# Performance work log

Hardware: AMD Instinct MI355X
Metric: run time of the kernel (lower is better)

## Reference

```python
import jax, jax.numpy as jnp
import numpy as np

N = 50000      # nodes
E = 800000     # edges (before self-loops)
F_IN = 128     # num_node_features
H = 4          # heads
C = 32         # graph_hidden_channels (per head)
HC = H * C     # 128
NHID = 512
NOUT = 768
G = 256        # graphs in batch
NEG_SLOPE = 0.2


def setup_inputs() -> dict:
    key = jax.random.key(0)
    ks = jax.random.split(key, 32)
    s = 0.05
    inp = {
        "x": jax.random.normal(ks[0], (N, F_IN), jnp.float32),
        "edge_index": jax.random.randint(ks[1], (2, E), 0, N, jnp.int64),
        "batch": jnp.sort(jax.random.randint(ks[2], (N,), 0, G, jnp.int64)),
    }
    dims = [F_IN, HC, HC]
    k = 3
    for i, din in enumerate(dims, start=1):
        inp[f"w{i}"] = jax.random.normal(ks[k], (din, HC), jnp.float32) * s; k += 1
        inp[f"as{i}"] = jax.random.normal(ks[k], (H, C), jnp.float32) * s; k += 1
        inp[f"ad{i}"] = jax.random.normal(ks[k], (H, C), jnp.float32) * s; k += 1
        inp[f"b{i}"] = jnp.zeros((HC,), jnp.float32)
        inp[f"sk{i}w"] = jax.random.normal(ks[k], (din, HC), jnp.float32) * s; k += 1
        inp[f"sk{i}b"] = jnp.zeros((HC,), jnp.float32)
    inp["m1w"] = jax.random.normal(ks[k], (HC, NHID), jnp.float32) * s; k += 1
    inp["m1b"] = jnp.zeros((NHID,), jnp.float32)
    inp["m2w"] = jax.random.normal(ks[k], (NHID, NOUT), jnp.float32) * s
    inp["m2b"] = jnp.zeros((NOUT,), jnp.float32)
    return inp


def _gat_conv(x, src, dst, W, a_src, a_dst, b):
    # x: [N, din]; src/dst: [E+N] (self-loops included)
    n = x.shape[0]
    h = (x @ W).reshape(n, H, C)                       # [N, H, C]
    e_src = jnp.sum(h * a_src, axis=-1)                # [N, H]
    e_dst = jnp.sum(h * a_dst, axis=-1)                # [N, H]
    e = jax.nn.leaky_relu(e_src[src] + e_dst[dst], NEG_SLOPE)  # [E', H]
    m = jax.ops.segment_max(e, dst, num_segments=n)    # segment softmax (stable)
    ex = jnp.exp(e - m[dst])
    z = jax.ops.segment_sum(ex, dst, num_segments=n)
    alpha = ex / z[dst]                                # [E', H]
    out = jax.ops.segment_sum(alpha[:, :, None] * h[src], dst, num_segments=n)
    return out.reshape(n, HC) + b


def reference(x, edge_index, batch,
              w1, as1, ad1, b1, sk1w, sk1b,
              w2, as2, ad2, b2, sk2w, sk2b,
              w3, as3, ad3, b3, sk3w, sk3b,
              m1w, m1b, m2w, m2b):
    n = x.shape[0]
    loops = jnp.arange(n, dtype=edge_index.dtype)
    src = jnp.concatenate([edge_index[0], loops])      # PyG add_self_loops=True
    dst = jnp.concatenate([edge_index[1], loops])

    h = jax.nn.relu(x @ sk1w + sk1b + _gat_conv(x, src, dst, w1, as1, ad1, b1))
    h = jax.nn.relu(h @ sk2w + sk2b + _gat_conv(h, src, dst, w2, as2, ad2, b2))
    h = jax.nn.relu(h @ sk3w + sk3b + _gat_conv(h, src, dst, w3, as3, ad3, b3))

    pooled = jax.ops.segment_max(h, batch, num_segments=G)  # global_max_pool
    pooled = jnp.where(jnp.isfinite(pooled), pooled, 0.0)   # guard empty graphs
    out = jax.nn.relu(pooled @ m1w + m1b)
    out = out @ m2w + m2b
    return out
```

## Files before the change

kernel.cpp:

```cpp
#include <hip/hip_runtime.h>
#include <hip/hip_bf16.h>
#include <math.h>

#define NN 50000
#define EE 800000
#define EPE 850000
#define HCC 128
#define GGR 256
#define NHIDD 512
#define NOUTD 768
#define CHUNK 256
#define CPAD (CHUNK + 8)
#define SCAN_NBLK ((NN + 1023) / 1024)
#define MBLK ((NN + 63) / 64)
#define NPAD 50176
#define NREP 8
#define NPART (NN / 8)

typedef __attribute__((ext_vector_type(8))) short bf16x8;
typedef __attribute__((ext_vector_type(4))) float f32x4;

__device__ __forceinline__ void atomicMaxF(float* addr, float v) {
    if (v >= 0.f) atomicMax(reinterpret_cast<int*>(addr), __float_as_int(v));
    else atomicMin(reinterpret_cast<unsigned int*>(addr), __float_as_uint(v));
}

__device__ __forceinline__ float lrelu(float x) { return x > 0.f ? x : 0.2f * x; }

__device__ __forceinline__ ushort f2bf(float f) {
    unsigned u = __float_as_uint(f);
    unsigned r = (u + 0x7fffu + ((u >> 16) & 1u)) >> 16;
    return (ushort)r;
}
__device__ __forceinline__ float bf2f(ushort b) {
    return __uint_as_float(((unsigned)b) << 16);
}

__global__ void conv_x(const float* __restrict__ X, ushort* __restrict__ Xb) {
    int i = blockIdx.x * 256 + threadIdx.x;
    if (i < NN * HCC / 4) {
        float4 v = reinterpret_cast<const float4*>(X)[i];
        ushort4 o;
        o.x = f2bf(v.x); o.y = f2bf(v.y); o.z = f2bf(v.z); o.w = f2bf(v.w);
        reinterpret_cast<ushort4*>(Xb)[i] = o;
    }
}

__global__ void conv_w(const float* __restrict__ W, const float* __restrict__ SKW,
                       ushort* __restrict__ Wt) {
    int i = blockIdx.x * 256 + threadIdx.x;
    if (i >= 256 * 128) return;
    int n = i >> 7, k = i & 127;
    float v = (n < 128) ? W[(size_t)k * 128 + n] : SKW[(size_t)k * 128 + (n - 128)];
    Wt[i] = f2bf(v);
}

__global__ void hist_zero8(int* __restrict__ cnt8) {
    int i = blockIdx.x * 256 + threadIdx.x;
    if (i < NREP * NPAD) cnt8[i] = 0;
}

__global__ void hist8(const int* __restrict__ ei, int* __restrict__ cnt8) {
    int e = blockIdx.x * 256 + threadIdx.x;
    if (e >= EPE) return;
    int rep = blockIdx.x & 7;
    int d = (e < EE) ? ei[EE + e] : e - EE;
    atomicAdd(&cnt8[rep * NPAD + d], 1);
}

__global__ __launch_bounds__(256) void scan_partial(const int* __restrict__ cnt8,
                                                    int* __restrict__ excl,
                                                    int* __restrict__ blocksums)
{
    __shared__ int s[256];
    const int b = blockIdx.x, t = threadIdx.x;
    const int idx = b * 1024 + t * 4;
    int a[4] = {0, 0, 0, 0};
    #pragma unroll
    for (int j = 0; j < 4; ++j) {
        if (idx + j < NN) {
            int tot = 0;
            #pragma unroll
            for (int r = 0; r < NREP; ++r) tot += cnt8[r * NPAD + idx + j];
            a[j] = tot;
        }
    }
    int sum4 = a[0] + a[1] + a[2] + a[3];
    s[t] = sum4;
    __syncthreads();
    #pragma unroll
    for (int off = 1; off < 256; off <<= 1) {
        int add = (t >= off) ? s[t - off] : 0;
        __syncthreads();
        s[t] += add;
        __syncthreads();
    }
    int e0 = s[t] - sum4;
    if (idx + 0 < NN) excl[idx + 0] = e0;
    if (idx + 1 < NN) excl[idx + 1] = e0 + a[0];
    if (idx + 2 < NN) excl[idx + 2] = e0 + a[0] + a[1];
    if (idx + 3 < NN) excl[idx + 3] = e0 + a[0] + a[1] + a[2];
    if (t == 255) blocksums[b] = s[255];
}

__global__ __launch_bounds__(64) void scan_sums(int* __restrict__ blocksums,
                                                int* __restrict__ blockoffs,
                                                int* __restrict__ row_start)
{
    __shared__ int s[64];
    int t = threadIdx.x;
    int v = (t < SCAN_NBLK) ? blocksums[t] : 0;
    s[t] = v;
    __syncthreads();
    #pragma unroll
    for (int off = 1; off < 64; off <<= 1) {
        int add = (t >= off) ? s[t - off] : 0;
        __syncthreads();
        s[t] += add;
        __syncthreads();
    }
    if (t < SCAN_NBLK) blockoffs[t] = s[t] - v;
    if (t == 63) row_start[NN] = s[63];
}

__global__ void scan_add(const int* __restrict__ excl, const int* __restrict__ blockoffs,
                         int* __restrict__ row_start, int* __restrict__ cursor)
{
    int i = blockIdx.x * 256 + threadIdx.x;
    if (i >= NN) return;
    int v = excl[i] + blockoffs[i >> 10];
    row_start[i] = v;
    cursor[i] = v;
}

__global__ __launch_bounds__(256) void scatter_part(const int* __restrict__ ei,
                                                    int* __restrict__ cursor,
                                                    int* __restrict__ csr_src)
{
    const int p = blockIdx.x & 7;
    const int q = blockIdx.x >> 3;
    const int nq = gridDim.x >> 3;
    const int lo = p * NPART, hi = lo + NPART;
    const int stride = nq * 256;
    for (int e = q * 256 + threadIdx.x; e < EE; e += stride) {
        int d = ei[EE + e];
        if (d >= lo && d < hi) {
            int s = ei[e];
            int pos = atomicAdd(&cursor[d], 1);
            csr_src[pos] = s;
        }
    }
    for (int i = q * 256 + threadIdx.x; i < NPART; i += stride) {
        int d = lo + i;
        int pos = atomicAdd(&cursor[d], 1);
        csr_src[pos] = d;
    }
}

__global__ __launch_bounds__(256) void gemm_mfma(
    const ushort* __restrict__ Xb,
    const ushort* __restrict__ Wt,
    const float* __restrict__ skb, const float* __restrict__ bb,
    const float* __restrict__ as_, const float* __restrict__ ad_,
    ushort* __restrict__ Hout, float* __restrict__ Agg,
    float* __restrict__ esrc, float* __restrict__ edst)
{
    __shared__ ushort Xs[64 * 128];
    __shared__ float sh_es[64][4], sh_ed[64][4];
    const int r0 = blockIdx.x * 64;
    const int tid = threadIdx.x;
    const int w = tid >> 6;
    const int l = tid & 63;
    const int lm = l & 15;
    const int lk = l >> 4;

    #pragma unroll
    for (int it = 0; it < 4; ++it) {
        int slot = it * 256 + tid;
        int row = slot >> 4;
        int bc = (slot & 15) << 4;
        int n = r0 + row;
        bf16x8 v = (bf16x8)(short)0;
        if (n < NN) v = *reinterpret_cast<const bf16x8*>(Xb + (size_t)n * 128 + (bc >> 1));
        *reinterpret_cast<bf16x8*>(reinterpret_cast<char*>(Xs) + row * 256 + (bc ^ ((row & 7) << 4))) = v;
    }
    __syncthreads();

    f32x4 acc[4][4];
    #pragma unroll
    for (int nb = 0; nb < 4; ++nb)
        #pragma unroll
        for (int rf = 0; rf < 4; ++rf)
            acc[nb][rf] = (f32x4){0.f, 0.f, 0.f, 0.f};

    #pragma unroll
    for (int ks = 0; ks < 4; ++ks) {
        bf16x8 a[4];
        #pragma unroll
        for (int rf = 0; rf < 4; ++rf) {
            int row = rf * 16 + lm;
            int bc = (ks * 32 + lk * 8) * 2;
            a[rf] = *reinterpret_cast<const bf16x8*>(
                reinterpret_cast<const char*>(Xs) + row * 256 + (bc ^ ((row & 7) << 4)));
        }
        #pragma unroll
        for (int nb = 0; nb < 4; ++nb) {
            int ncol = (w * 4 + nb) * 16 + lm;
            bf16x8 b = *reinterpret_cast<const bf16x8*>(Wt + (size_t)ncol * 128 + ks * 32 + lk * 8);
            #pragma unroll
            for (int rf = 0; rf < 4; ++rf)
                acc[nb][rf] = __builtin_amdgcn_mfma_f32_16x16x32_bf16(a[rf], b, acc[nb][rf], 0, 0, 0);
        }
    }

    if (w < 2) {
        float asv[4], adv[4];
        #pragma unroll
        for (int nb = 0; nb < 4; ++nb) {
            int ncol = (w * 4 + nb) * 16 + lm;
            asv[nb] = as_[ncol];
            adv[nb] = ad_[ncol];
        }
        #pragma unroll
        for (int rf = 0; rf < 4; ++rf) {
            #pragma unroll
            for (int r = 0; r < 4; ++r) {
                int nl = rf * 16 + lk * 4 + r;
                int n = r0 + nl;
                float es0 = 0.f, es1 = 0.f, ed0 = 0.f, ed1 = 0.f;
                #pragma unroll
                for (int nb = 0; nb < 4; ++nb) {
                    float v = acc[nb][rf][r];
                    int ncol = (w * 4 + nb) * 16 + lm;
                    if (n < NN) Hout[(size_t)n * 128 + ncol] = f2bf(v);
                    if (nb < 2) { es0 = fmaf(v, asv[nb], es0); ed0 = fmaf(v, adv[nb], ed0); }
                    else        { es1 = fmaf(v, asv[nb], es1); ed1 = fmaf(v, adv[nb], ed1); }
                }
                #pragma unroll
                for (int m = 1; m < 16; m <<= 1) {
                    es0 += __shfl_xor(es0, m); ed0 += __shfl_xor(ed0, m);
                    es1 += __shfl_xor(es1, m); ed1 += __shfl_xor(ed1, m);
                }
                if (lm == 0) {
                    sh_es[nl][w * 2 + 0] = es0; sh_ed[nl][w * 2 + 0] = ed0;
                    sh_es[nl][w * 2 + 1] = es1; sh_ed[nl][w * 2 + 1] = ed1;
                }
            }
        }
    } else {
        #pragma unroll
        for (int nb = 0; nb < 4; ++nb) {
            int ncol = (w * 4 + nb) * 16 + lm;
            int c = ncol - 128;
            #pragma unroll
            for (int rf = 0; rf < 4; ++rf) {
                #pragma unroll
                for (int r = 0; r < 4; ++r) {
                    int n = r0 + rf * 16 + lk * 4 + r;
                    if (n >= NN) continue;
                    Agg[(size_t)n * 128 + c] = acc[nb][rf][r] + skb[c] + bb[c];
                }
            }
        }
    }
    __syncthreads();
    if (tid < 256) {
        int nl = tid >> 2, hd = tid & 3;
        int n = r0 + nl;
        if (n < NN) {
            esrc[n * 4 + hd] = sh_es[nl][hd];
            edst[n * 4 + hd] = sh_ed[nl][hd];
        }
    }
}

__global__ __launch_bounds__(128) void gat_aggr(
    const int* __restrict__ row_start, const int* __restrict__ csr_src,
    const float* __restrict__ esrc, const float* __restrict__ edst,
    const ushort* __restrict__ Hb, const float* __restrict__ skipagg,
    ushort* __restrict__ outbuf)
{
    __shared__ int   lsrc[CHUNK];
    __shared__ float lw[4][CPAD];
    __shared__ float shsc[4];
    __shared__ float accbuf[8][HCC];
    const int d = blockIdx.x;
    const int t = threadIdx.x;
    const int hd = t >> 5;
    const int l = t & 31;
    const int slot = t >> 4;
    const int cg = t & 15;
    const int c0 = cg * 8;
    const int ghd = cg >> 2;
    const int r0 = row_start[d], r1 = row_start[d + 1];
    const float4 edv = *reinterpret_cast<const float4*>(edst + (size_t)d * 4);
    float acc[8] = {0.f, 0.f, 0.f, 0.f, 0.f, 0.f, 0.f, 0.f};
    float m_h = -INFINITY, z_h = 0.f;

    for (int base = r0; base < r1; base += CHUNK) {
        const int nc = min(CHUNK, r1 - base);
        __syncthreads();
        for (int i = t; i < nc; i += 128) {
            int s = csr_src[base + i];
            lsrc[i] = s;
            float4 ev = *reinterpret_cast<const float4*>(esrc + (size_t)s * 4);
            lw[0][i] = lrelu(ev.x + edv.x);
            lw[1][i] = lrelu(ev.y + edv.y);
            lw[2][i] = lrelu(ev.z + edv.z);
            lw[3][i] = lrelu(ev.w + edv.w);
        }
        __syncthreads();
        float mx = m_h;
        for (int i = l; i < nc; i += 32) mx = fmaxf(mx, lw[hd][i]);
        #pragma unroll
        for (int off = 16; off > 0; off >>= 1) mx = fmaxf(mx, __shfl_xor(mx, off, 32));
        float sc = __expf(m_h - mx);
        float zp = 0.f;
        for (int i = l; i < nc; i += 32) {
            float w = __expf(lw[hd][i] - mx);
            lw[hd][i] = w;
            zp += w;
        }
        #pragma unroll
        for (int off = 16; off > 0; off >>= 1) zp += __shfl_xor(zp, off, 32);
        z_h = z_h * sc + zp;
        m_h = mx;
        if (l == 0) shsc[hd] = sc;
        __syncthreads();
        float scg = shsc[ghd];
        #pragma unroll
        for (int j = 0; j < 8; ++j) acc[j] *= scg;
        for (int i = slot; i < nc; i += 8) {
            int s = lsrc[i];
            float wgt = lw[ghd][i];
            bf16x8 row = *reinterpret_cast<const bf16x8*>(Hb + (size_t)s * 128 + c0);
            #pragma unroll
            for (int j = 0; j < 8; ++j)
                acc[j] = fmaf(wgt, bf2f((ushort)row[j]), acc[j]);
        }
    }
    #pragma unroll
    for (int j = 0; j < 8; ++j) accbuf[slot][c0 + j] = acc[j];
    __syncthreads();
    float tot = 0.f;
    #pragma unroll
    for (int s = 0; s < 8; ++s) tot += accbuf[s][t];
    float res = skipagg[(size_t)d * 128 + t] + tot / z_h;
    outbuf[(size_t)d * 128 + t] = f2bf(fmaxf(res, 0.f));
}

__global__ void pool_init(float* __restrict__ pooled) {
    int i = blockIdx.x * 256 + threadIdx.x;
    if (i < GGR * HCC) pooled[i] = -INFINITY;
}

__global__ __launch_bounds__(256) void pool_max_sorted(
    const ushort* __restrict__ xf, const int* __restrict__ batch,
    float* __restrict__ pooled)
{
    __shared__ int gb[32];
    const int n0 = blockIdx.x * 32;
    const int t = threadIdx.x;
    if (t < 32) gb[t] = (n0 + t < NN) ? batch[n0 + t] : -1;
    __syncthreads();
    const int c = t & 127;
    const int half = t >> 7;
    int curg = -1;
    float curv = -INFINITY;
    #pragma unroll 4
    for (int i = 0; i < 16; ++i) {
        int n = n0 + half * 16 + i;
        if (n >= NN) break;
        int g = gb[half * 16 + i];
        float v = bf2f(xf[(size_t)n * 128 + c]);
        if (g != curg) {
            if (curg >= 0) atomicMaxF(&pooled[curg * 128 + c], curv);
            curg = g; curv = v;
        } else {
            curv = fmaxf(curv, v);
        }
    }
    if (curg >= 0) atomicMaxF(&pooled[curg * 128 + c], curv);
}

__global__ __launch_bounds__(512) void mlp1(const float* __restrict__ pooled,
                                            const float* __restrict__ w,
                                            const float* __restrict__ bias,
                                            float* __restrict__ hid)
{
    __shared__ float xs[128];
    int g = blockIdx.x, t = threadIdx.x;
    if (t < 128) {
        float v = pooled[g * 128 + t];
        if (!isfinite(v)) v = 0.f;
        xs[t] = v;
    }
    __syncthreads();
    float acc = 0.f;
    #pragma unroll 8
    for (int k = 0; k < 128; ++k) acc += xs[k] * w[(size_t)k * NHIDD + t];
    hid[(size_t)g * NHIDD + t] = fmaxf(acc + bias[t], 0.f);
}

__global__ __launch_bounds__(768) void mlp2(const float* __restrict__ hid,
                                            const float* __restrict__ w,
                                            const float* __restrict__ bias,
                                            float* __restrict__ out)
{
    __shared__ float xs[NHIDD];
    int g = blockIdx.x, t = threadIdx.x;
    if (t < NHIDD) xs[t] = hid[(size_t)g * NHIDD + t];
    __syncthreads();
    float acc = 0.f;
    #pragma unroll 8
    for (int k = 0; k < NHIDD; ++k) acc += xs[k] * w[(size_t)k * NOUTD + t];
    out[(size_t)g * NOUTD + t] = acc + bias[t];
}

extern "C" void kernel_launch(void* const* d_in, const int* in_sizes, int n_in,
                              void* d_out, int out_size, void* d_ws, size_t ws_size,
                              hipStream_t stream)
{
    const float* x = (const float*)d_in[0];
    const int* ei = (const int*)d_in[1];
    const int* batch = (const int*)d_in[2];
    const float* W[3]   = {(const float*)d_in[3],  (const float*)d_in[9],  (const float*)d_in[15]};
    const float* AS[3]  = {(const float*)d_in[4],  (const float*)d_in[10], (const float*)d_in[16]};
    const float* AD[3]  = {(const float*)d_in[5],  (const float*)d_in[11], (const float*)d_in[17]};
    const float* B[3]   = {(const float*)d_in[6],  (const float*)d_in[12], (const float*)d_in[18]};
    const float* SKW[3] = {(const float*)d_in[7],  (const float*)d_in[13], (const float*)d_in[19]};
    const float* SKB[3] = {(const float*)d_in[8],  (const float*)d_in[14], (const float*)d_in[20]};
    const float* m1w = (const float*)d_in[21];
    const float* m1b = (const float*)d_in[22];
    const float* m2w = (const float*)d_in[23];
    const float* m2b = (const float*)d_in[24];
    float* out = (float*)d_out;

    float* p = (float*)d_ws;
    ushort* bufA = (ushort*)p; p += (size_t)NN * HCC / 2;
    ushort* bufB = (ushort*)p; p += (size_t)NN * HCC / 2;
    ushort* xb   = (ushort*)p; p += (size_t)NN * HCC / 2;
    ushort* hbuf = (ushort*)p; p += (size_t)NN * HCC / 2;
    ushort* wt3  = (ushort*)p; p += 3 * 256 * 128 / 2;
    float* agg  = p; p += (size_t)NN * HCC;
    float* esrc = p; p += NN * 4;
    float* edst = p; p += NN * 4;
    float* pooled = p; p += GGR * HCC;
    float* hidden = p; p += GGR * NHIDD;
    int* cnt8      = (int*)p; p += NREP * NPAD;
    int* cursor    = (int*)p; p += NN;
    int* excl      = (int*)p; p += NN;
    int* row_start = (int*)p; p += NN + 4;
    int* csr_src   = (int*)p; p += EPE;
    int* blocksums = (int*)p; p += 64;
    int* blockoffs = (int*)p; p += 64;

    conv_x<<<(NN * HCC / 4 + 255) / 256, 256, 0, stream>>>(x, xb);
    for (int l = 0; l < 3; ++l)
        conv_w<<<(256 * 128 + 255) / 256, 256, 0, stream>>>(W[l], SKW[l], wt3 + l * 256 * 128);

    hist_zero8<<<(NREP * NPAD + 255) / 256, 256, 0, stream>>>(cnt8);
    hist8<<<(EPE + 255) / 256, 256, 0, stream>>>(ei, cnt8);
    scan_partial<<<SCAN_NBLK, 256, 0, stream>>>(cnt8, excl, blocksums);
    scan_sums<<<1, 64, 0, stream>>>(blocksums, blockoffs, row_start);
    scan_add<<<(NN + 255) / 256, 256, 0, stream>>>(excl, blockoffs, row_start, cursor);
    scatter_part<<<1024, 256, 0, stream>>>(ei, cursor, csr_src);

    const ushort* cur = xb;
    ushort* outs[3] = {bufA, bufB, bufA};
    for (int l = 0; l < 3; ++l) {
        gemm_mfma<<<MBLK, 256, 0, stream>>>(cur, wt3 + l * 256 * 128, SKB[l], B[l],
                                            AS[l], AD[l], hbuf, agg, esrc, edst);
        gat_aggr<<<NN, 128, 0, stream>>>(row_start, csr_src, esrc, edst, hbuf, agg, outs[l]);
        cur = outs[l];
    }
    pool_init<<<(GGR * HCC) / 256, 256, 0, stream>>>(pooled);
    pool_max_sorted<<<(NN + 31) / 32, 256, 0, stream>>>(cur, batch, pooled);
    mlp1<<<GGR, NHIDD, 0, stream>>>(pooled, m1w, m1b, hidden);
    mlp2<<<GGR, NOUTD, 0, stream>>>(hidden, m2w, m2b, out);
}
```

Before: 494.1 us.

## Process one destination node per wavefront in GAT aggregation using shuffles

Replaces the block-per-node GAT aggregation with a wave-per-node kernel, four nodes per 256-thread block. The online softmax is computed in registers over 64-edge chunks with wavefront shuffle reductions, replacing shared-memory staging and block barriers. Edge sources and weights are broadcast with shuffles, and partial sums are reduced across slots with xor shuffles. This removes LDS traffic and __syncthreads, and stops launching 50000 small blocks. The cost is only 4 edges in flight per wave in the gather loop, against 8 before.

Result: slower. 513.0 us (+3.8%).

```diff
diff --git a/kernel.cpp b/kernel.cpp
--- a/kernel.cpp
+++ b/kernel.cpp
@@ -9,8 +9,6 @@
 #define GGR 256
 #define NHIDD 512
 #define NOUTD 768
-#define CHUNK 256
-#define CPAD (CHUNK + 8)
 #define SCAN_NBLK ((NN + 1023) / 1024)
 #define MBLK ((NN + 63) / 64)
 #define NPAD 50176
@@ -34,6 +32,12 @@
 }
 __device__ __forceinline__ float bf2f(ushort b) {
     return __uint_as_float(((unsigned)b) << 16);
+}
+
+__device__ __forceinline__ float sel4(int k, float a0, float a1, float a2, float a3) {
+    float lo = (k & 1) ? a1 : a0;
+    float hi = (k & 1) ? a3 : a2;
+    return (k & 2) ? hi : lo;
 }
 
 __global__ void conv_x(const float* __restrict__ X, ushort* __restrict__ Xb) {
@@ -274,79 +278,99 @@
     }
 }
 
-__global__ __launch_bounds__(128) void gat_aggr(
+__global__ __launch_bounds__(256) void gat_aggr_wave(
     const int* __restrict__ row_start, const int* __restrict__ csr_src,
     const float* __restrict__ esrc, const float* __restrict__ edst,
     const ushort* __restrict__ Hb, const float* __restrict__ skipagg,
     ushort* __restrict__ outbuf)
 {
-    __shared__ int   lsrc[CHUNK];
-    __shared__ float lw[4][CPAD];
-    __shared__ float shsc[4];
-    __shared__ float accbuf[8][HCC];
-    const int d = blockIdx.x;
     const int t = threadIdx.x;
-    const int hd = t >> 5;
-    const int l = t & 31;
-    const int slot = t >> 4;
-    const int cg = t & 15;
+    const int d = blockIdx.x * 4 + (t >> 6);
+    if (d >= NN) return;
+    const int l = t & 63;
+    const int slot = l >> 4;
+    const int cg = l & 15;
     const int c0 = cg * 8;
     const int ghd = cg >> 2;
     const int r0 = row_start[d], r1 = row_start[d + 1];
     const float4 edv = *reinterpret_cast<const float4*>(edst + (size_t)d * 4);
+
     float acc[8] = {0.f, 0.f, 0.f, 0.f, 0.f, 0.f, 0.f, 0.f};
-    float m_h = -INFINITY, z_h = 0.f;
-
-    for (int base = r0; base < r1; base += CHUNK) {
-        const int nc = min(CHUNK, r1 - base);
-        __syncthreads();
-        for (int i = t; i < nc; i += 128) {
-            int s = csr_src[base + i];
-            lsrc[i] = s;
-            float4 ev = *reinterpret_cast<const float4*>(esrc + (size_t)s * 4);
-            lw[0][i] = lrelu(ev.x + edv.x);
-            lw[1][i] = lrelu(ev.y + edv.y);
-            lw[2][i] = lrelu(ev.z + edv.z);
-            lw[3][i] = lrelu(ev.w + edv.w);
-        }
-        __syncthreads();
-        float mx = m_h;
-        for (int i = l; i < nc; i += 32) mx = fmaxf(mx, lw[hd][i]);
-        #pragma unroll
-        for (int off = 16; off > 0; off >>= 1) mx = fmaxf(mx, __shfl_xor(mx, off, 32));
-        float sc = __expf(m_h - mx);
-        float zp = 0.f;
-        for (int i = l; i < nc; i += 32) {
-            float w = __expf(lw[hd][i] - mx);
-            lw[hd][i] = w;
-            zp += w;
-        }
-        #pragma unroll
-        for (int off = 16; off > 0; off >>= 1) zp += __shfl_xor(zp, off, 32);
-        z_h = z_h * sc + zp;
-        m_h = mx;
-        if (l == 0) shsc[hd] = sc;
-        __syncthreads();
-        float scg = shsc[ghd];
+    float m0 = -INFINITY, m1 = -INFINITY, m2 = -INFINITY, m3 = -INFINITY;
+    float z0 = 0.f, z1 = 0.f, z2 = 0.f, z3 = 0.f;
+
+    for (int base = r0; base < r1; base += 64) {
+        const int nc = min(64, r1 - base);
+        int sreg = 0;
+        float g0 = -INFINITY, g1 = -INFINITY, g2 = -INFINITY, g3 = -INFINITY;
+        if (l < nc) {
+            sreg = csr_src[base + l];
+            float4 ev = *reinterpret_cast<const float4*>(esrc + (size_t)sreg * 4);
+            g0 = lrelu(ev.x + edv.x);
+            g1 = lrelu(ev.y + edv.y);
+            g2 = lrelu(ev.z + edv.z);
+            g3 = lrelu(ev.w + edv.w);
+        }
+        float x0 = fmaxf(m0, g0), x1 = fmaxf(m1, g1), x2 = fmaxf(m2, g2), x3 = fmaxf(m3, g3);
+        #pragma unroll
+        for (int off = 1; off < 64; off <<= 1) {
+            x0 = fmaxf(x0, __shfl_xor(x0, off));
+            x1 = fmaxf(x1, __shfl_xor(x1, off));
+            x2 = fmaxf(x2, __shfl_xor(x2, off));
+            x3 = fmaxf(x3, __shfl_xor(x3, off));
+        }
+        float sc0 = __expf(m0 - x0), sc1 = __expf(m1 - x1);
+        float sc2 = __expf(m2 - x2), sc3 = __expf(m3 - x3);
+        float w0 = __expf(g0 - x0), w1 = __expf(g1 - x1);
+        float w2 = __expf(g2 - x2), w3 = __expf(g3 - x3);
+        float p0 = w0, p1 = w1, p2 = w2, p3 = w3;
+        #pragma unroll
+        for (int off = 1; off < 64; off <<= 1) {
+            p0 += __shfl_xor(p0, off);
+            p1 += __shfl_xor(p1, off);
+            p2 += __shfl_xor(p2, off);
+            p3 += __shfl_xor(p3, off);
+        }
+        z0 = z0 * sc0 + p0; z1 = z1 * sc1 + p1;
+        z2 = z2 * sc2 + p2; z3 = z3 * sc3 + p3;
+        m0 = x0; m1 = x1; m2 = x2; m3 = x3;
+        float scg = sel4(ghd, sc0, sc1, sc2, sc3);
         #pragma unroll
         for (int j = 0; j < 8; ++j) acc[j] *= scg;
-        for (int i = slot; i < nc; i += 8) {
-            int s = lsrc[i];
-            float wgt = lw[ghd][i];
-            bf16x8 row = *reinterpret_cast<const bf16x8*>(Hb + (size_t)s * 128 + c0);
-            #pragma unroll
-            for (int j = 0; j < 8; ++j)
-                acc[j] = fmaf(wgt, bf2f((ushort)row[j]), acc[j]);
-        }
-    }
-    #pragma unroll
-    for (int j = 0; j < 8; ++j) accbuf[slot][c0 + j] = acc[j];
-    __syncthreads();
-    float tot = 0.f;
-    #pragma unroll
-    for (int s = 0; s < 8; ++s) tot += accbuf[s][t];
-    float res = skipagg[(size_t)d * 128 + t] + tot / z_h;
-    outbuf[(size_t)d * 128 + t] = f2bf(fmaxf(res, 0.f));
+        for (int i0 = 0; i0 < nc; i0 += 4) {
+            int e = i0 + slot;
+            int s_e = __shfl(sreg, e);
+            float u0 = __shfl(w0, e), u1 = __shfl(w1, e);
+            float u2 = __shfl(w2, e), u3 = __shfl(w3, e);
+            if (e < nc) {
+                float wgt = sel4(ghd, u0, u1, u2, u3);
+                bf16x8 row = *reinterpret_cast<const bf16x8*>(Hb + (size_t)s_e * 128 + c0);
+                #pragma unroll
+                for (int j = 0; j < 8; ++j)
+                    acc[j] = fmaf(wgt, bf2f((ushort)row[j]), acc[j]);
+            }
+        }
+    }
+    #pragma unroll
+    for (int j = 0; j < 8; ++j) {
+        acc[j] += __shfl_xor(acc[j], 16);
+        acc[j] += __shfl_xor(acc[j], 32);
+    }
+    if (slot == 0) {
+        float zi = 1.f / sel4(ghd, z0, z1, z2, z3);
+        ushort4 o0, o1;
+        const float* sk = skipagg + (size_t)d * 128 + c0;
+        o0.x = f2bf(fmaxf(sk[0] + acc[0] * zi, 0.f));
+        o0.y = f2bf(fmaxf(sk[1] + acc[1] * zi, 0.f));
+        o0.z = f2bf(fmaxf(sk[2] + acc[2] * zi, 0.f));
+        o0.w = f2bf(fmaxf(sk[3] + acc[3] * zi, 0.f));
+        o1.x = f2bf(fmaxf(sk[4] + acc[4] * zi, 0.f));
+        o1.y = f2bf(fmaxf(sk[5] + acc[5] * zi, 0.f));
+        o1.z = f2bf(fmaxf(sk[6] + acc[6] * zi, 0.f));
+        o1.w = f2bf(fmaxf(sk[7] + acc[7] * zi, 0.f));
+        *reinterpret_cast<ushort4*>(outbuf + (size_t)d * 128 + c0) = o0;
+        *reinterpret_cast<ushort4*>(outbuf + (size_t)d * 128 + c0 + 4) = o1;
+    }
 }
 
 __global__ void pool_init(float* __restrict__ pooled) {
@@ -471,7 +495,8 @@
     for (int l = 0; l < 3; ++l) {
         gemm_mfma<<<MBLK, 256, 0, stream>>>(cur, wt3 + l * 256 * 128, SKB[l], B[l],
                                             AS[l], AD[l], hbuf, agg, esrc, edst);
-        gat_aggr<<<NN, 128, 0, stream>>>(row_start, csr_src, esrc, edst, hbuf, agg, outs[l]);
+        gat_aggr_wave<<<(NN + 3) / 4, 256, 0, stream>>>(row_start, csr_src, esrc, edst,
+                                                        hbuf, agg, outs[l]);
         cur = outs[l];
     }
     pool_init<<<(GGR * HCC) / 256, 256, 0, stream>>>(pooled);
```

## Fuse prep kernels into one launch, fuse MLP, and store CSR sources as ushort

Applied to the files above, without the earlier changes.

Merges x conversion, three weight transposes, histogram zeroing and pool init into a single prep kernel. The two MLP layers are fused into one kernel that keeps the hidden vector in shared memory. CSR source indices are stored as 16-bit ushort to halve index traffic in gat_aggr. The aim is fewer launches and less memory traffic. The 16-bit indices are wrong for this size: node ids reach 49999, which does not fit in the signed 16-bit range but does fit unsigned 16-bit (max 65535), so ushort is actually fine.

Measured after the change: 492.5 us. No clear change (-0.3%).

```diff
diff --git a/kernel.cpp b/kernel.cpp
--- a/kernel.cpp
+++ b/kernel.cpp
@@ -36,28 +36,51 @@
     return __uint_as_float(((unsigned)b) << 16);
 }
 
-__global__ void conv_x(const float* __restrict__ X, ushort* __restrict__ Xb) {
-    int i = blockIdx.x * 256 + threadIdx.x;
-    if (i < NN * HCC / 4) {
+#define PB_X 6250
+#define PB_W 128
+#define PB_C 1568
+#define PB_P 128
+#define PREP_BLOCKS (PB_X + 3 * PB_W + PB_C + PB_P)
+
+__global__ __launch_bounds__(256) void prep(
+    const float* __restrict__ X, ushort* __restrict__ Xb,
+    const float* __restrict__ W0, const float* __restrict__ SKW0,
+    const float* __restrict__ W1, const float* __restrict__ SKW1,
+    const float* __restrict__ W2, const float* __restrict__ SKW2,
+    ushort* __restrict__ wt3, int* __restrict__ cnt8, float* __restrict__ pooled)
+{
+    int b = blockIdx.x;
+    int t = threadIdx.x;
+    if (b < PB_X) {
+        int i = b * 256 + t;
         float4 v = reinterpret_cast<const float4*>(X)[i];
         ushort4 o;
         o.x = f2bf(v.x); o.y = f2bf(v.y); o.z = f2bf(v.z); o.w = f2bf(v.w);
         reinterpret_cast<ushort4*>(Xb)[i] = o;
-    }
-}
-
-__global__ void conv_w(const float* __restrict__ W, const float* __restrict__ SKW,
-                       ushort* __restrict__ Wt) {
-    int i = blockIdx.x * 256 + threadIdx.x;
-    if (i >= 256 * 128) return;
-    int n = i >> 7, k = i & 127;
-    float v = (n < 128) ? W[(size_t)k * 128 + n] : SKW[(size_t)k * 128 + (n - 128)];
-    Wt[i] = f2bf(v);
-}
-
-__global__ void hist_zero8(int* __restrict__ cnt8) {
-    int i = blockIdx.x * 256 + threadIdx.x;
-    if (i < NREP * NPAD) cnt8[i] = 0;
+        return;
+    }
+    b -= PB_X;
+    if (b < 3 * PB_W) {
+        int l = b / PB_W;
+        int i = (b % PB_W) * 256 + t;
+        int n = i >> 7, k = i & 127;
+        const float* W = (l == 0) ? W0 : (l == 1) ? W1 : W2;
+        const float* SKW = (l == 0) ? SKW0 : (l == 1) ? SKW1 : SKW2;
+        float v = (n < 128) ? W[(size_t)k * 128 + n] : SKW[(size_t)k * 128 + (n - 128)];
+        wt3[l * 256 * 128 + i] = f2bf(v);
+        return;
+    }
+    b -= 3 * PB_W;
+    if (b < PB_C) {
+        int i = b * 256 + t;
+        if (i < NREP * NPAD) cnt8[i] = 0;
+        return;
+    }
+    b -= PB_C;
+    {
+        int i = b * 256 + t;
+        if (i < GGR * HCC) pooled[i] = -INFINITY;
+    }
 }
 
 __global__ void hist8(const int* __restrict__ ei, int* __restrict__ cnt8) {
@@ -135,7 +158,7 @@
 
 __global__ __launch_bounds__(256) void scatter_part(const int* __restrict__ ei,
                                                     int* __restrict__ cursor,
-                                                    int* __restrict__ csr_src)
+                                                    ushort* __restrict__ csr_src)
 {
     const int p = blockIdx.x & 7;
     const int q = blockIdx.x >> 3;
@@ -147,13 +170,13 @@
         if (d >= lo && d < hi) {
             int s = ei[e];
             int pos = atomicAdd(&cursor[d], 1);
-            csr_src[pos] = s;
+            csr_src[pos] = (ushort)s;
         }
     }
     for (int i = q * 256 + threadIdx.x; i < NPART; i += stride) {
         int d = lo + i;
         int pos = atomicAdd(&cursor[d], 1);
-        csr_src[pos] = d;
+        csr_src[pos] = (ushort)d;
     }
 }
 
@@ -275,7 +298,7 @@
 }
 
 __global__ __launch_bounds__(128) void gat_aggr(
-    const int* __restrict__ row_start, const int* __restrict__ csr_src,
+    const int* __restrict__ row_start, const ushort* __restrict__ csr_src,
     const float* __restrict__ esrc, const float* __restrict__ edst,
     const ushort* __restrict__ Hb, const float* __restrict__ skipagg,
     ushort* __restrict__ outbuf)
@@ -301,7 +324,7 @@
         const int nc = min(CHUNK, r1 - base);
         __syncthreads();
         for (int i = t; i < nc; i += 128) {
-            int s = csr_src[base + i];
+            int s = (int)csr_src[base + i];
             lsrc[i] = s;
             float4 ev = *reinterpret_cast<const float4*>(esrc + (size_t)s * 4);
             lw[0][i] = lrelu(ev.x + edv.x);
@@ -347,11 +370,6 @@
     for (int s = 0; s < 8; ++s) tot += accbuf[s][t];
     float res = skipagg[(size_t)d * 128 + t] + tot / z_h;
     outbuf[(size_t)d * 128 + t] = f2bf(fmaxf(res, 0.f));
-}
-
-__global__ void pool_init(float* __restrict__ pooled) {
-    int i = blockIdx.x * 256 + threadIdx.x;
-    if (i < GGR * HCC) pooled[i] = -INFINITY;
 }
 
 __global__ __launch_bounds__(256) void pool_max_sorted(
@@ -383,12 +401,14 @@
     if (curg >= 0) atomicMaxF(&pooled[curg * 128 + c], curv);
 }
 
-__global__ __launch_bounds__(512) void mlp1(const float* __restrict__ pooled,
-                                            const float* __restrict__ w,
-                                            const float* __restrict__ bias,
-                                            float* __restrict__ hid)
+__global__ __launch_bounds__(768) void mlp_fused(
+    const float* __restrict__ pooled,
+    const float* __restrict__ w1, const float* __restrict__ b1,
+    const float* __restrict__ w2, const float* __restrict__ b2,
+    float* __restrict__ out)
 {
     __shared__ float xs[128];
+    __shared__ float hs[NHIDD];
     int g = blockIdx.x, t = threadIdx.x;
     if (t < 128) {
         float v = pooled[g * 128 + t];
@@ -396,25 +416,17 @@
         xs[t] = v;
     }
     __syncthreads();
+    if (t < NHIDD) {
+        float acc = 0.f;
+        #pragma unroll 8
+        for (int k = 0; k < 128; ++k) acc += xs[k] * w1[(size_t)k * NHIDD + t];
+        hs[t] = fmaxf(acc + b1[t], 0.f);
+    }
+    __syncthreads();
     float acc = 0.f;
     #pragma unroll 8
-    for (int k = 0; k < 128; ++k) acc += xs[k] * w[(size_t)k * NHIDD + t];
-    hid[(size_t)g * NHIDD + t] = fmaxf(acc + bias[t], 0.f);
-}
-
-__global__ __launch_bounds__(768) void mlp2(const float* __restrict__ hid,
-                                            const float* __restrict__ w,
-                                            const float* __restrict__ bias,
-                                            float* __restrict__ out)
-{
-    __shared__ float xs[NHIDD];
-    int g = blockIdx.x, t = threadIdx.x;
-    if (t < NHIDD) xs[t] = hid[(size_t)g * NHIDD + t];
-    __syncthreads();
-    float acc = 0.f;
-    #pragma unroll 8
-    for (int k = 0; k < NHIDD; ++k) acc += xs[k] * w[(size_t)k * NOUTD + t];
-    out[(size_t)g * NOUTD + t] = acc + bias[t];
+    for (int k = 0; k < NHIDD; ++k) acc += hs[k] * w2[(size_t)k * NOUTD + t];
+    out[(size_t)g * NOUTD + t] = acc + b2[t];
 }
 
 extern "C" void kernel_launch(void* const* d_in, const int* in_sizes, int n_in,
@@ -446,20 +458,16 @@
     float* esrc = p; p += NN * 4;
     float* edst = p; p += NN * 4;
     float* pooled = p; p += GGR * HCC;
-    float* hidden = p; p += GGR * NHIDD;
     int* cnt8      = (int*)p; p += NREP * NPAD;
     int* cursor    = (int*)p; p += NN;
     int* excl      = (int*)p; p += NN;
     int* row_start = (int*)p; p += NN + 4;
-    int* csr_src   = (int*)p; p += EPE;
+    ushort* csr_src = (ushort*)p; p += (EPE + 1) / 2;
     int* blocksums = (int*)p; p += 64;
     int* blockoffs = (int*)p; p += 64;
 
-    conv_x<<<(NN * HCC / 4 + 255) / 256, 256, 0, stream>>>(x, xb);
-    for (int l = 0; l < 3; ++l)
-        conv_w<<<(256 * 128 + 255) / 256, 256, 0, stream>>>(W[l], SKW[l], wt3 + l * 256 * 128);
-
-    hist_zero8<<<(NREP * NPAD + 255) / 256, 256, 0, stream>>>(cnt8);
+    prep<<<PREP_BLOCKS, 256, 0, stream>>>(x, xb, W[0], SKW[0], W[1], SKW[1], W[2], SKW[2],
+                                          wt3, cnt8, pooled);
     hist8<<<(EPE + 255) / 256, 256, 0, stream>>>(ei, cnt8);
     scan_partial<<<SCAN_NBLK, 256, 0, stream>>>(cnt8, excl, blocksums);
     scan_sums<<<1, 64, 0, stream>>>(blocksums, blockoffs, row_start);
@@ -474,8 +482,6 @@
         gat_aggr<<<NN, 128, 0, stream>>>(row_start, csr_src, esrc, edst, hbuf, agg, outs[l]);
         cur = outs[l];
     }
-    pool_init<<<(GGR * HCC) / 256, 256, 0, stream>>>(pooled);
     pool_max_sorted<<<(NN + 31) / 32, 256, 0, stream>>>(cur, batch, pooled);
-    mlp1<<<GGR, NHIDD, 0, stream>>>(pooled, m1w, m1b, hidden);
-    mlp2<<<GGR, NOUTD, 0, stream>>>(hidden, m2w, m2b, out);
-}
+    mlp_fused<<<GGR, NOUTD, 0, stream>>>(pooled, m1w, m1b, m2w, m2b, out);
+}
```
